# Kernel tuning notes

Measured on AMD Instinct MI355X. Metric: run time of the kernel, lower is better.

## Reference

```python
import jax, jax.numpy as jnp
import numpy as np

DIM = 768
HID = 3072
E_SPEC = 4
E_SHARED = 2
TOP_K = 2
LN_EPS = 1e-5


def _expert_stack_params(key, n_experts):
    k1, k2, k3, k4 = jax.random.split(key, 4)
    s1 = 1.0 / np.sqrt(DIM)
    s2 = 1.0 / np.sqrt(HID)
    return {
        'w1': jax.random.uniform(k1, (n_experts, DIM, HID), minval=-s1, maxval=s1, dtype=jnp.float32),
        'b1': jax.random.uniform(k2, (n_experts, HID), minval=-s1, maxval=s1, dtype=jnp.float32),
        'w2': jax.random.uniform(k3, (n_experts, HID, DIM), minval=-s2, maxval=s2, dtype=jnp.float32),
        'b2': jax.random.uniform(k4, (n_experts, DIM), minval=-s2, maxval=s2, dtype=jnp.float32),
    }


def setup_inputs() -> dict:
    key = jax.random.key(0)
    ks = jax.random.split(key, 8)
    B, N = 64, 196
    s = 1.0 / np.sqrt(DIM)
    spec = _expert_stack_params(ks[1], E_SPEC)
    shared = _expert_stack_params(ks[2], E_SHARED)
    return {
        'x': jax.random.normal(ks[0], (B, N, DIM), dtype=jnp.float32),
        'ln_gamma': jnp.ones((DIM,), jnp.float32),
        'ln_beta': jnp.zeros((DIM,), jnp.float32),
        'spec_router_w': jax.random.uniform(ks[3], (DIM, E_SPEC), minval=-s, maxval=s, dtype=jnp.float32),
        'spec_router_b': jnp.zeros((E_SPEC,), jnp.float32),
        'spec_w1': spec['w1'], 'spec_b1': spec['b1'], 'spec_w2': spec['w2'], 'spec_b2': spec['b2'],
        'shared_router_w': jax.random.uniform(ks[4], (DIM, E_SHARED), minval=-s, maxval=s, dtype=jnp.float32),
        'shared_router_b': jnp.zeros((E_SHARED,), jnp.float32),
        'sh_w1': shared['w1'], 'sh_b1': shared['b1'], 'sh_w2': shared['w2'], 'sh_b2': shared['b2'],
    }


def _all_experts(x, w1, b1, w2, b2):
    # x: [B,N,D]; w1: [E,D,H] -> out: [B,N,E,D]
    h = jnp.einsum('bnd,edh->bneh', x, w1) + b1
    h = jax.nn.gelu(h, approximate=False)  # torch nn.GELU default is exact
    return jnp.einsum('bneh,ehd->bned', h, w2) + b2


def reference(x, ln_gamma, ln_beta,
              spec_router_w, spec_router_b, spec_w1, spec_b1, spec_w2, spec_b2,
              shared_router_w, shared_router_b, sh_w1, sh_b1, sh_w2, sh_b2):
    # LayerNorm
    mu = jnp.mean(x, axis=-1, keepdims=True)
    var = jnp.mean(jnp.square(x - mu), axis=-1, keepdims=True)
    xn = (x - mu) * jax.lax.rsqrt(var + LN_EPS) * ln_gamma + ln_beta

    # Specific-expert branch: dense all-expert compute, then top-k gather (faithful)
    spec_logits = xn @ spec_router_w + spec_router_b            # [B,N,E]
    spec_probs = jax.nn.softmax(spec_logits, axis=-1)
    topk_probs, topk_idx = jax.lax.top_k(spec_probs, TOP_K)    # [B,N,K]
    spec_out_all = _all_experts(xn, spec_w1, spec_b1, spec_w2, spec_b2)  # [B,N,E,D]
    sel = jnp.take_along_axis(spec_out_all, topk_idx[..., None], axis=2)  # [B,N,K,D]
    specific_out = jnp.sum(topk_probs[..., None] * sel, axis=2)

    # Shared-expert branch: softmax-weighted sum over all experts
    sh_logits = xn @ shared_router_w + shared_router_b          # [B,N,Es]
    sh_probs = jax.nn.softmax(sh_logits, axis=-1)
    sh_out_all = _all_experts(xn, sh_w1, sh_b1, sh_w2, sh_b2)   # [B,N,Es,D]
    shared_out = jnp.einsum('bne,bned->bnd', sh_probs, sh_out_all)

    out = specific_out + shared_out
    return (out, spec_logits, spec_probs, topk_idx, topk_probs, sh_logits, sh_probs)
```

## Files before the change

kernel.cpp:

```cpp
#include <hip/hip_runtime.h>
#include <hip/hip_bf16.h>
#include <math.h>

#define NTOK 12544
#define DIM 768
#define HID 3072
#define NTILE_MAX 102
#define NSLOT_MAX (NTILE_MAX * 256)
#define NSDT 49
#define NVT (NTILE_MAX + 2 * NSDT)
#define NBKT 64
#define BKTCAP 256
#define LDSB 131072

typedef __hip_bfloat16 bf16;
typedef __attribute__((ext_vector_type(8))) short short8v;
typedef __attribute__((ext_vector_type(4))) float f32x4;

#define GPTR(p)  ((const __attribute__((address_space(1))) void*)(p))
#define LDSPTR(p) ((__attribute__((address_space(3))) void*)(p))

__global__ __launch_bounds__(256) void conv_all_kernel(
    const float* __restrict__ spec_w1, const float* __restrict__ sh_w1,
    const float* __restrict__ spec_w2, const float* __restrict__ sh_w2,
    bf16* __restrict__ w1t, bf16* __restrict__ w2t,
    int* __restrict__ cnt2, int* __restrict__ slot_tok, float* __restrict__ slot_gate) {
    int z = blockIdx.y;
    int ti = blockIdx.x;
    int t = threadIdx.x;
    if (z == 0) {
        if (ti == 0) cnt2[t] = 0;
        if (ti < NTILE_MAX) {
            int s = ti * 256 + t;
            slot_tok[s] = 0; slot_gate[s] = 0.0f;
        }
    }
    const float* src; bf16* dst; int R, C, tr, tc;
    if (z < 6) {
        R = DIM; C = HID;
        src = (z < 4) ? spec_w1 + (size_t)z * R * C : sh_w1 + (size_t)(z - 4) * R * C;
        dst = w1t + (size_t)z * R * C;
        tr = ti % 12; tc = ti / 12;
    } else {
        int e = z - 6;
        R = HID; C = DIM;
        src = (e < 4) ? spec_w2 + (size_t)e * R * C : sh_w2 + (size_t)(e - 4) * R * C;
        dst = w2t + (size_t)e * R * C;
        tr = ti % 48; tc = ti / 48;
    }
    __shared__ float tile[64][65];
    int r0 = tr * 64, c0 = tc * 64;
    int lr = t >> 4, lc = (t & 15) * 4;
    #pragma unroll
    for (int ii = 0; ii < 4; ++ii) {
        float4 v = *(const float4*)&src[(size_t)(r0 + lr + 16 * ii) * C + c0 + lc];
        tile[lc + 0][lr + 16 * ii] = v.x;
        tile[lc + 1][lr + 16 * ii] = v.y;
        tile[lc + 2][lr + 16 * ii] = v.z;
        tile[lc + 3][lr + 16 * ii] = v.w;
    }
    __syncthreads();
    int oc = t >> 4, orr = (t & 15) * 4;
    #pragma unroll
    for (int ii = 0; ii < 4; ++ii) {
        union { ushort4 u4; bf16 h[4]; } pk;
        #pragma unroll
        for (int k = 0; k < 4; ++k)
            pk.h[k] = __float2bfloat16(tile[oc + 16 * ii][orr + k]);
        *(ushort4*)&dst[(size_t)(c0 + oc + 16 * ii) * R + r0 + orr] = pk.u4;
    }
}

__global__ void router_ln_kernel(const float* __restrict__ x,
                                 const float* __restrict__ lng, const float* __restrict__ lnb,
                                 const float* __restrict__ srw, const float* __restrict__ srb,
                                 const float* __restrict__ shw, const float* __restrict__ shb,
                                 bf16* __restrict__ xnb,
                                 float* __restrict__ spec_logits, float* __restrict__ spec_probs,
                                 float* __restrict__ topk_idx, float* __restrict__ topk_probs,
                                 float* __restrict__ sh_logits, float* __restrict__ sh_probs,
                                 float* __restrict__ gates,
                                 int* __restrict__ cnt2, int* __restrict__ tok2,
                                 float* __restrict__ gate2) {
    int t = blockIdx.x * 4 + (threadIdx.x >> 6);
    int bucket = blockIdx.x & (NBKT - 1);
    int lane = threadIdx.x & 63;
    const float* xr = x + (size_t)t * DIM;
    bf16* xb = xnb + (size_t)t * DIM;
    float v[12];
    float s = 0.0f;
    #pragma unroll
    for (int i = 0; i < 6; ++i) {
        float2 xv = *(const float2*)&xr[lane * 2 + 128 * i];
        v[2 * i] = xv.x; v[2 * i + 1] = xv.y;
        s += xv.x + xv.y;
    }
    #pragma unroll
    for (int o = 32; o > 0; o >>= 1) s += __shfl_xor(s, o, 64);
    float mean = s * (1.0f / 768.0f);
    float sq = 0.0f;
    #pragma unroll
    for (int i = 0; i < 12; ++i) { float d = v[i] - mean; sq += d * d; }
    #pragma unroll
    for (int o = 32; o > 0; o >>= 1) sq += __shfl_xor(sq, o, 64);
    float rstd = rsqrtf(sq * (1.0f / 768.0f) + 1e-5f);

    float acc[6] = {0, 0, 0, 0, 0, 0};
    #pragma unroll
    for (int i = 0; i < 6; ++i) {
        int d0 = lane * 2 + 128 * i;
        float xn0 = (v[2 * i]     - mean) * rstd * lng[d0]     + lnb[d0];
        float xn1 = (v[2 * i + 1] - mean) * rstd * lng[d0 + 1] + lnb[d0 + 1];
        union { unsigned u; bf16 h[2]; } pk;
        pk.h[0] = __float2bfloat16(xn0);
        pk.h[1] = __float2bfloat16(xn1);
        *(unsigned*)&xb[d0] = pk.u;
        float4 a = *(const float4*)&srw[d0 * 4];
        float4 b = *(const float4*)&srw[d0 * 4 + 4];
        acc[0] += xn0 * a.x + xn1 * b.x;
        acc[1] += xn0 * a.y + xn1 * b.y;
        acc[2] += xn0 * a.z + xn1 * b.z;
        acc[3] += xn0 * a.w + xn1 * b.w;
        float4 sw = *(const float4*)&shw[d0 * 2];
        acc[4] += xn0 * sw.x + xn1 * sw.z;
        acc[5] += xn0 * sw.y + xn1 * sw.w;
    }
    #pragma unroll
    for (int j = 0; j < 6; ++j) {
        #pragma unroll
        for (int o = 32; o > 0; o >>= 1) acc[j] += __shfl_xor(acc[j], o, 64);
    }
    if (lane == 0) {
        float l[4];
        #pragma unroll
        for (int j = 0; j < 4; ++j) l[j] = acc[j] + srb[j];
        float m = fmaxf(fmaxf(l[0], l[1]), fmaxf(l[2], l[3]));
        float e[4], ssum = 0.0f;
        #pragma unroll
        for (int j = 0; j < 4; ++j) { e[j] = expf(l[j] - m); ssum += e[j]; }
        float inv = 1.0f / ssum;
        float p[4];
        #pragma unroll
        for (int j = 0; j < 4; ++j) p[j] = e[j] * inv;
        int i0 = 0;
        for (int j = 1; j < 4; ++j) if (p[j] > p[i0]) i0 = j;
        int i1 = -1;
        for (int j = 0; j < 4; ++j) {
            if (j == i0) continue;
            if (i1 < 0 || p[j] > p[i1]) i1 = j;
        }
        float sl0 = acc[4] + shb[0], sl1 = acc[5] + shb[1];
        float sm = fmaxf(sl0, sl1);
        float se0 = expf(sl0 - sm), se1 = expf(sl1 - sm);
        float sinv = 1.0f / (se0 + se1);
        float sp0 = se0 * sinv, sp1 = se1 * sinv;

        #pragma unroll
        for (int j = 0; j < 4; ++j) {
            spec_logits[t * 4 + j] = l[j];
            spec_probs[t * 4 + j]  = p[j];
        }
        topk_idx[t * 2 + 0]   = (float)i0;
        topk_idx[t * 2 + 1]   = (float)i1;
        topk_probs[t * 2 + 0] = p[i0];
        topk_probs[t * 2 + 1] = p[i1];
        sh_logits[t * 2 + 0]  = sl0;
        sh_logits[t * 2 + 1]  = sl1;
        sh_probs[t * 2 + 0]   = sp0;
        sh_probs[t * 2 + 1]   = sp1;
        float gg[6] = {0, 0, 0, 0, sp0, sp1};
        gg[i0] = p[i0];
        gg[i1] = p[i1];
        #pragma unroll
        for (int j = 0; j < 6; ++j) gates[t * 6 + j] = gg[j];
        int c0 = i0 * NBKT + bucket;
        int pos0 = atomicAdd(&cnt2[c0], 1);
        tok2[c0 * BKTCAP + pos0]  = t * 2 + 0;
        gate2[c0 * BKTCAP + pos0] = p[i0];
        int c1 = i1 * NBKT + bucket;
        int pos1 = atomicAdd(&cnt2[c1], 1);
        tok2[c1 * BKTCAP + pos1]  = t * 2 + 1;
        gate2[c1 * BKTCAP + pos1] = p[i1];
    }
}

__global__ void plan_kernel(const int* __restrict__ cnt2, int* __restrict__ e_of_tile,
                            const int* __restrict__ tok2, const float* __restrict__ gate2,
                            int* __restrict__ slot_tok, float* __restrict__ slot_gate,
                            int* __restrict__ back) {
    __shared__ int sbase[4 * NBKT];
    __shared__ int offsE[5];
    __shared__ int etot[4];
    int tid = threadIdx.x, lane = tid & 63, wid = tid >> 6;
    int c = cnt2[wid * NBKT + lane];
    int inc = c;
    #pragma unroll
    for (int o = 1; o < 64; o <<= 1) {
        int tv = __shfl_up(inc, o, 64);
        if (lane >= o) inc += tv;
    }
    int exc = inc - c;
    if (lane == 63) etot[wid] = inc;
    __syncthreads();
    if (tid == 0) {
        int o = 0;
        for (int e = 0; e < 4; ++e) { offsE[e] = o; o += (etot[e] + 255) & ~255; }
        offsE[4] = o;
    }
    __syncthreads();
    sbase[tid] = offsE[wid] + exc;
    for (int idx = tid; idx < NTILE_MAX; idx += 256) {
        int s0 = idx * 256, e = -1;
        for (int j = 0; j < 4; ++j)
            if (s0 >= offsE[j] && s0 < offsE[j + 1]) e = j;
        e_of_tile[idx] = e;
    }
    __syncthreads();
    int bs = sbase[tid];
    int cc = cnt2[tid];
    for (int i = 0; i < cc; ++i) {
        int gs = bs + i;
        int tk = tok2[tid * BKTCAP + i];
        slot_tok[gs] = tk >> 1;
        slot_gate[gs] = gate2[tid * BKTCAP + i];
        back[tk] = gs;
    }
}


__device__ __forceinline__ int swz(int off) {
    return off ^ (((off >> 8) & 1) << 4) ^ (((off >> 9) & 1) << 5);
}

__device__ __forceinline__ void stage2(bf16* lds, int base_elems, int wid,
                                       const bf16* s0, const bf16* s1) {
    __builtin_amdgcn_global_load_lds(GPTR(s0), LDSPTR(lds + base_elems + wid * 512), 16, 0, 0);
    __builtin_amdgcn_global_load_lds(GPTR(s1), LDSPTR(lds + base_elems + 4096 + wid * 512), 16, 0, 0);
}

__device__ __forceinline__ void read_a4(const bf16* lds, int buf, int ks, int wm, int mh,
                                        int lane, short8v a[4]) {
    const char* base = (const char*)lds + buf * 32768 + ks * 16384;
    #pragma unroll
    for (int i = 0; i < 4; ++i) {
        int off = (wm * 128 + mh * 64 + i * 16 + (lane & 15)) * 64 + ((lane >> 4) * 16);
        a[i] = *(const short8v*)(base + swz(off));
    }
}

__device__ __forceinline__ void read_b4(const bf16* lds, int buf, int ks, int wn,
                                        int lane, short8v b[4]) {
    const char* base = (const char*)lds + 65536 + buf * 32768 + ks * 16384;
    #pragma unroll
    for (int j = 0; j < 4; ++j) {
        int off = (wn * 64 + j * 16 + (lane & 15)) * 64 + ((lane >> 4) * 16);
        b[j] = *(const short8v*)(base + swz(off));
    }
}

__device__ __forceinline__ void mfma16(const short8v a[4], const short8v b[4], f32x4 (*am)[4]) {
    #pragma unroll
    for (int i = 0; i < 4; ++i)
        #pragma unroll
        for (int j = 0; j < 4; ++j)
            am[i][j] = __builtin_amdgcn_mfma_f32_16x16x32_bf16(a[i], b[j], am[i][j], 0, 0, 0);
}

#define BARRIER() __builtin_amdgcn_s_barrier()
#define VMCNT4() asm volatile("s_waitcnt vmcnt(4)" ::: "memory")
#define VMCNT0() asm volatile("s_waitcnt vmcnt(0)" ::: "memory")

template<int NT>
__device__ __forceinline__ void kloop8p(bf16* lds, const bf16* a0, const bf16* a1,
                                        const bf16* b0, const bf16* b1,
                                        int wm, int wn, int wid, int lane,
                                        f32x4 acc[8][4]) {
    stage2(lds, 0, wid, a0, a1);
    stage2(lds, 32768, wid, b0, b1);
    stage2(lds, 8192, wid, a0 + 32, a1 + 32);
    stage2(lds, 32768 + 8192, wid, b0 + 32, b1 + 32);
    VMCNT4();
    BARRIER();
    for (int t = 0; t < NT; ++t) {
        int buf = t & 1, nb = buf ^ 1;
        bool pre = (t + 1 < NT);
        short8v af[4], bfv[4];
        if (pre) stage2(lds, nb * 16384, wid, a0 + (t + 1) * 64, a1 + (t + 1) * 64);
        read_a4(lds, buf, 0, wm, 0, lane, af);
        read_b4(lds, buf, 0, wn, lane, bfv);
        BARRIER();
        __builtin_amdgcn_s_setprio(1);
        mfma16(af, bfv, &acc[0]);
        __builtin_amdgcn_s_setprio(0);
        BARRIER();
        if (pre) stage2(lds, 32768 + nb * 16384, wid, b0 + (t + 1) * 64, b1 + (t + 1) * 64);
        read_a4(lds, buf, 0, wm, 1, lane, af);
        BARRIER();
        __builtin_amdgcn_s_setprio(1);
        mfma16(af, bfv, &acc[4]);
        __builtin_amdgcn_s_setprio(0);
        if (pre) VMCNT4(); else VMCNT0();
        BARRIER();
        if (pre) stage2(lds, nb * 16384 + 8192, wid, a0 + (t + 1) * 64 + 32, a1 + (t + 1) * 64 + 32);
        read_a4(lds, buf, 1, wm, 0, lane, af);
        read_b4(lds, buf, 1, wn, lane, bfv);
        BARRIER();
        __builtin_amdgcn_s_setprio(1);
        mfma16(af, bfv, &acc[0]);
        __builtin_amdgcn_s_setprio(0);
        BARRIER();
        if (pre) stage2(lds, 32768 + nb * 16384 + 8192, wid, b0 + (t + 1) * 64 + 32, b1 + (t + 1) * 64 + 32);
        read_a4(lds, buf, 1, wm, 1, lane, af);
        BARRIER();
        __builtin_amdgcn_s_setprio(1);
        mfma16(af, bfv, &acc[4]);
        __builtin_amdgcn_s_setprio(0);
        if (pre) VMCNT4();
        BARRIER();
    }
}

__device__ __forceinline__ float gelu_exact(float v) {
    return 0.5f * v * (1.0f + erff(v * 0.70710678118654752f));
}

__global__ __launch_bounds__(512, 2) void gemm1_8p(
    const bf16* __restrict__ xnb, const bf16* __restrict__ w1t,
    const float* __restrict__ spec_b1, const float* __restrict__ sh_b1,
    const int* __restrict__ e_of_tile, const int* __restrict__ slot_tok,
    bf16* __restrict__ Hbuf, int y_base) {
    extern __shared__ bf16 lds[];
    int y = blockIdx.y + y_base;
    int tid = threadIdx.x, wid = tid >> 6, lane = tid & 63;
    int wm = wid >> 2, wn = wid & 3;
    int P0c = tid, P1c = 512 + tid;
    int L0 = P0c ^ ((P0c >> 4) & 1) ^ (((P0c >> 5) & 1) << 1);
    int L1 = P1c ^ ((P1c >> 4) & 1) ^ (((P1c >> 5) & 1) << 1);
    int r0 = L0 >> 2, c0 = (L0 & 3) * 8;
    int r1 = L1 >> 2, c1 = (L1 & 3) * 8;

    const bf16 *a0, *a1, *Bw;
    const float* bias;
    if (y < NTILE_MAX) {
        int e = e_of_tile[y];
        if (e < 0) return;
        a0 = xnb + (size_t)slot_tok[y * 256 + r0] * DIM + c0;
        a1 = xnb + (size_t)slot_tok[y * 256 + r1] * DIM + c1;
        Bw = w1t + (size_t)e * HID * DIM;
        bias = spec_b1 + (size_t)e * HID;
    } else {
        int ys = y - NTILE_MAX;
        int z = ys / NSDT, ry = ys % NSDT;
        a0 = xnb + (size_t)(ry * 256 + r0) * DIM + c0;
        a1 = xnb + (size_t)(ry * 256 + r1) * DIM + c1;
        Bw = w1t + (size_t)(4 + z) * HID * DIM;
        bias = sh_b1 + (size_t)z * HID;
    }
    const bf16* b0 = Bw + (size_t)(blockIdx.x * 256 + r0) * DIM + c0;
    const bf16* b1 = Bw + (size_t)(blockIdx.x * 256 + r1) * DIM + c1;

    f32x4 acc[8][4] = {};
    kloop8p<DIM / 64>(lds, a0, a1, b0, b1, wm, wn, wid, lane, acc);

    bf16* hb = Hbuf + (size_t)blockIdx.y * 256 * HID;
    int fr = lane & 15, fq = lane >> 4;
    int cb = blockIdx.x * 256 + wn * 64;
    #pragma unroll
    for (int j = 0; j < 4; ++j) {
        int col = cb + j * 16 + fr;
        float bv = bias[col];
        #pragma unroll
        for (int ii = 0; ii < 8; ++ii) {
            #pragma unroll
            for (int rr = 0; rr < 4; ++rr) {
                int row = wm * 128 + (ii >> 2) * 64 + (ii & 3) * 16 + fq * 4 + rr;
                hb[(size_t)row * HID + col] = __float2bfloat16(gelu_exact(acc[ii][j][rr] + bv));
            }
        }
    }
}

__global__ __launch_bounds__(512, 2) void gemm2_8p(
    const bf16* __restrict__ Hbuf, const bf16* __restrict__ w2t,
    const float* __restrict__ spec_b2, const float* __restrict__ sh_b2,
    const int* __restrict__ e_of_tile, const float* __restrict__ slot_gate,
    const float* __restrict__ sh_probs,
    bf16* __restrict__ spec_g, bf16* __restrict__ shg, int y_base) {
    extern __shared__ bf16 lds[];
    int y = blockIdx.y + y_base;
    int tid = threadIdx.x, wid = tid >> 6, lane = tid & 63;
    int wm = wid >> 2, wn = wid & 3;
    int P0c = tid, P1c = 512 + tid;
    int L0 = P0c ^ ((P0c >> 4) & 1) ^ (((P0c >> 5) & 1) << 1);
    int L1 = P1c ^ ((P1c >> 4) & 1) ^ (((P1c >> 5) & 1) << 1);
    int r0 = L0 >> 2, c0 = (L0 & 3) * 8;
    int r1 = L1 >> 2, c1 = (L1 & 3) * 8;

    const bf16 *Bw;
    const float* bias;
    bf16* obase;
    bool grouped = (y < NTILE_MAX);
    int z = 0, ry = 0;
    if (grouped) {
        int e = e_of_tile[y];
        if (e < 0) return;
        Bw = w2t + (size_t)e * DIM * HID;
        bias = spec_b2 + (size_t)e * DIM;
        obase = spec_g + (size_t)y * 256 * DIM;
    } else {
        int ys = y - NTILE_MAX;
        z = ys / NSDT; ry = ys % NSDT;
        Bw = w2t + (size_t)(4 + z) * DIM * HID;
        bias = sh_b2 + (size_t)z * DIM;
        obase = shg + (size_t)(z * NTOK + ry * 256) * DIM;
    }
    const bf16* Ah = Hbuf + (size_t)blockIdx.y * 256 * HID;
    const bf16* a0 = Ah + (size_t)r0 * HID + c0;
    const bf16* a1 = Ah + (size_t)r1 * HID + c1;
    const bf16* b0 = Bw + (size_t)(blockIdx.x * 256 + r0) * HID + c0;
    const bf16* b1 = Bw + (size_t)(blockIdx.x * 256 + r1) * HID + c1;

    f32x4 acc[8][4] = {};
    kloop8p<HID / 64>(lds, a0, a1, b0, b1, wm, wn, wid, lane, acc);

    int fr = lane & 15, fq = lane >> 4;
    int cb = blockIdx.x * 256 + wn * 64;
    #pragma unroll
    for (int j = 0; j < 4; ++j) {
        int col = cb + j * 16 + fr;
        float bv = bias[col];
        #pragma unroll
        for (int ii = 0; ii < 8; ++ii) {
            #pragma unroll
            for (int rr = 0; rr < 4; ++rr) {
                int row = wm * 128 + (ii >> 2) * 64 + (ii & 3) * 16 + fq * 4 + rr;
                float g = grouped ? slot_gate[y * 256 + row]
                                  : sh_probs[(size_t)(ry * 256 + row) * 2 + z];
                obase[(size_t)row * DIM + col] = __float2bfloat16(g * (acc[ii][j][rr] + bv));
            }
        }
    }
}

__device__ __forceinline__ void stage_tile(const bf16* __restrict__ g, int ldg,
                                           bf16* lds, int tid) {
    int wave = tid >> 6, lane = tid & 63;
    #pragma unroll
    for (int q = 0; q < 2; ++q) {
        int chunk = wave * 2 + q;
        int row = chunk * 16 + (lane >> 2);
        int col = (lane & 3) * 8;
        __builtin_amdgcn_global_load_lds(GPTR(g + (size_t)row * ldg + col),
                                         LDSPTR(lds + chunk * 512), 16, 0, 0);
    }
}

__device__ __forceinline__ void mfma_step(const bf16* As, const bf16* Bs,
                                          int wr, int wc, int fr, int fq, f32x4 acc[4][4]) {
    short8v a[4], b[4];
    #pragma unroll
    for (int i = 0; i < 4; ++i) {
        a[i] = *(const short8v*)&As[(wr * 64 + i * 16 + fr) * 32 + fq * 8];
        b[i] = *(const short8v*)&Bs[(wc * 64 + i * 16 + fr) * 32 + fq * 8];
    }
    #pragma unroll
    for (int i = 0; i < 4; ++i)
        #pragma unroll
        for (int j = 0; j < 4; ++j)
            acc[i][j] = __builtin_amdgcn_mfma_f32_16x16x32_bf16(a[i], b[j], acc[i][j], 0, 0, 0);
}

__global__ __launch_bounds__(256) void gemm1_dense(
    const bf16* __restrict__ A, const bf16* __restrict__ BT,
    const float* __restrict__ bias, bf16* __restrict__ H) {
    __shared__ bf16 As[128 * 32];
    __shared__ bf16 Bs[128 * 32];
    int tid = threadIdx.x;
    int wid = tid >> 6, lane = tid & 63;
    int wr = wid >> 1, wc = wid & 1;
    int fr = lane & 15, fq = lane >> 4;
    const bf16* Ag = A + (size_t)(blockIdx.y * 128) * DIM;
    const bf16* Bg = BT + (size_t)(blockIdx.x * 128) * DIM;
    f32x4 acc[4][4] = {};
    for (int k0 = 0; k0 < DIM; k0 += 32) {
        stage_tile(Ag + k0, DIM, As, tid);
        stage_tile(Bg + k0, DIM, Bs, tid);
        __syncthreads();
        mfma_step(As, Bs, wr, wc, fr, fq, acc);
        __syncthreads();
    }
    int rbase = blockIdx.y * 128 + wr * 64;
    int cbase = blockIdx.x * 128 + wc * 64;
    #pragma unroll
    for (int j = 0; j < 4; ++j) {
        int col = cbase + j * 16 + fr;
        float bv = bias[col];
        #pragma unroll
        for (int i = 0; i < 4; ++i)
            #pragma unroll
            for (int r = 0; r < 4; ++r) {
                int row = rbase + i * 16 + fq * 4 + r;
                H[(size_t)row * HID + col] = __float2bfloat16(gelu_exact(acc[i][j][r] + bv));
            }
    }
}

__global__ __launch_bounds__(256) void gemm2_dense_out(
    const bf16* __restrict__ A, const bf16* __restrict__ BT,
    const float* __restrict__ bias, const float* __restrict__ gates,
    float* __restrict__ out, int gidx, int accum) {
    __shared__ bf16 As[128 * 32];
    __shared__ bf16 Bs[128 * 32];
    int tid = threadIdx.x;
    int wid = tid >> 6, lane = tid & 63;
    int wr = wid >> 1, wc = wid & 1;
    int fr = lane & 15, fq = lane >> 4;
    const bf16* Ag = A + (size_t)(blockIdx.y * 128) * HID;
    const bf16* Bg = BT + (size_t)(blockIdx.x * 128) * HID;
    f32x4 acc[4][4] = {};
    for (int k0 = 0; k0 < HID; k0 += 32) {
        stage_tile(Ag + k0, HID, As, tid);
        stage_tile(Bg + k0, HID, Bs, tid);
        __syncthreads();
        mfma_step(As, Bs, wr, wc, fr, fq, acc);
        __syncthreads();
    }
    int rbase = blockIdx.y * 128 + wr * 64;
    int cbase = blockIdx.x * 128 + wc * 64;
    #pragma unroll
    for (int j = 0; j < 4; ++j) {
        int col = cbase + j * 16 + fr;
        float bv = bias[col];
        #pragma unroll
        for (int i = 0; i < 4; ++i)
            #pragma unroll
            for (int r = 0; r < 4; ++r) {
                int row = rbase + i * 16 + fq * 4 + r;
                float g = gates[(size_t)row * 6 + gidx];
                float v = g * (acc[i][j][r] + bv);
                size_t idx = (size_t)row * DIM + col;
                out[idx] = accum ? out[idx] + v : v;
            }
    }
}

__global__ void combine_kernel(const bf16* __restrict__ spec_g, const bf16* __restrict__ shg,
                               const int* __restrict__ back, float* __restrict__ out) {
    int idx = blockIdx.x * 256 + threadIdx.x;
    int tok = idx / 96;
    int c = (idx % 96) * 8;
    int b0 = back[2 * tok], b1 = back[2 * tok + 1];
    short8v q0 = *(const short8v*)&spec_g[(size_t)b0 * DIM + c];
    short8v q1 = *(const short8v*)&spec_g[(size_t)b1 * DIM + c];
    short8v s0 = *(const short8v*)&shg[(size_t)tok * DIM + c];
    short8v s1 = *(const short8v*)&shg[(size_t)(NTOK + tok) * DIM + c];
    float o[8];
    #pragma unroll
    for (int k = 0; k < 8; ++k) {
        float f0 = __uint_as_float((unsigned)(unsigned short)q0[k] << 16);
        float f1 = __uint_as_float((unsigned)(unsigned short)q1[k] << 16);
        float f2 = __uint_as_float((unsigned)(unsigned short)s0[k] << 16);
        float f3 = __uint_as_float((unsigned)(unsigned short)s1[k] << 16);
        o[k] = f0 + f1 + f2 + f3;
    }
    float* op = out + (size_t)tok * DIM + c;
    *(float4*)(op)     = *(const float4*)(o);
    *(float4*)(op + 4) = *(const float4*)(o + 4);
}

static inline size_t align256(size_t x) { return (x + 255) & ~(size_t)255; }

extern "C" void kernel_launch(void* const* d_in, const int* in_sizes, int n_in,
                              void* d_out, int out_size, void* d_ws, size_t ws_size,
                              hipStream_t stream) {
    const float* x      = (const float*)d_in[0];
    const float* gamma  = (const float*)d_in[1];
    const float* beta   = (const float*)d_in[2];
    const float* srw    = (const float*)d_in[3];
    const float* srb    = (const float*)d_in[4];
    const float* spec_w1 = (const float*)d_in[5];
    const float* spec_b1 = (const float*)d_in[6];
    const float* spec_w2 = (const float*)d_in[7];
    const float* spec_b2 = (const float*)d_in[8];
    const float* shw    = (const float*)d_in[9];
    const float* shb    = (const float*)d_in[10];
    const float* sh_w1  = (const float*)d_in[11];
    const float* sh_b1  = (const float*)d_in[12];
    const float* sh_w2  = (const float*)d_in[13];
    const float* sh_b2  = (const float*)d_in[14];

    char* p = (char*)d_ws;
    size_t off = 0;
    bf16* xnb = (bf16*)(p + off);       off = align256(off + (size_t)NTOK * DIM * 2);
    bf16* w1t = (bf16*)(p + off);       off = align256(off + (size_t)6 * HID * DIM * 2);
    bf16* w2t = (bf16*)(p + off);       off = align256(off + (size_t)6 * DIM * HID * 2);
    int*  cnt2 = (int*)(p + off);       off = align256(off + (size_t)4 * NBKT * 4);
    float* gates = (float*)(p + off);   off = align256(off + (size_t)NTOK * 6 * 4);
    int*  tok2 = (int*)(p + off);       off = align256(off + (size_t)4 * NBKT * BKTCAP * 4);
    float* gate2 = (float*)(p + off);   off = align256(off + (size_t)4 * NBKT * BKTCAP * 4);
    int*  slot_tok = (int*)(p + off);   off = align256(off + (size_t)NSLOT_MAX * 4);
    float* slot_gate = (float*)(p + off); off = align256(off + (size_t)NSLOT_MAX * 4);
    int*  back = (int*)(p + off);       off = align256(off + (size_t)2 * NTOK * 4);
    int*  e_of_tile = (int*)(p + off);  off = align256(off + (size_t)NTILE_MAX * 4);
    bf16* spec_g = (bf16*)(p + off);    off = align256(off + (size_t)NSLOT_MAX * DIM * 2);
    bf16* shg   = (bf16*)(p + off);     off = align256(off + (size_t)2 * NTOK * DIM * 2);
    size_t fixed_end = off;
    bf16* Hbuf = (bf16*)(p + fixed_end);

    const size_t tile_bytes = (size_t)256 * HID * 2;
    size_t avail = (ws_size > fixed_end) ? (ws_size - fixed_end) : 0;
    int tcap = (int)(avail / tile_bytes);
    if (tcap > NVT) tcap = NVT;

    float* out         = (float*)d_out;
    float* spec_logits = out + (size_t)NTOK * DIM;
    float* spec_probs  = spec_logits + (size_t)NTOK * 4;
    float* topk_idx    = spec_probs  + (size_t)NTOK * 4;
    float* topk_probs  = topk_idx    + (size_t)NTOK * 2;
    float* sh_logits   = topk_probs  + (size_t)NTOK * 2;
    float* sh_probs    = sh_logits   + (size_t)NTOK * 2;

    conv_all_kernel<<<dim3(576, 12), 256, 0, stream>>>(
        spec_w1, sh_w1, spec_w2, sh_w2, w1t, w2t, cnt2, slot_tok, slot_gate);

    router_ln_kernel<<<NTOK / 4, 256, 0, stream>>>(x, gamma, beta, srw, srb, shw, shb, xnb,
                                                   spec_logits, spec_probs, topk_idx,
                                                   topk_probs, sh_logits, sh_probs, gates,
                                                   cnt2, tok2, gate2);

    if (tcap >= 16) {
        plan_kernel<<<1, 256, 0, stream>>>(cnt2, e_of_tile, tok2, gate2,
                                           slot_tok, slot_gate, back);
        for (int c0 = 0; c0 < NVT; c0 += tcap) {
            int n = NVT - c0 < tcap ? NVT - c0 : tcap;
            gemm1_8p<<<dim3(HID / 256, n), 512, LDSB, stream>>>(
                xnb, w1t, spec_b1, sh_b1, e_of_tile, slot_tok, Hbuf, c0);
            gemm2_8p<<<dim3(DIM / 256, n), 512, LDSB, stream>>>(
                Hbuf, w2t, spec_b2, sh_b2, e_of_tile, slot_gate, sh_probs,
                spec_g, shg, c0);
        }
        combine_kernel<<<NTOK * 96 / 256, 256, 0, stream>>>(spec_g, shg, back, out);
    } else {
        bf16* HB = spec_g;
        for (int e = 0; e < 6; ++e) {
            const bf16* w1p = w1t + (size_t)e * HID * DIM;
            const bf16* w2p = w2t + (size_t)e * DIM * HID;
            const float* b1p = (e < 4) ? spec_b1 + (size_t)e * HID : sh_b1 + (size_t)(e - 4) * HID;
            const float* b2p = (e < 4) ? spec_b2 + (size_t)e * DIM : sh_b2 + (size_t)(e - 4) * DIM;
            gemm1_dense<<<dim3(HID / 128, NTOK / 128), 256, 0, stream>>>(xnb, w1p, b1p, HB);
            gemm2_dense_out<<<dim3(DIM / 128, NTOK / 128), 256, 0, stream>>>(
                HB, w2p, b2p, gates, out, e, e > 0);
        }
    }
}
```

Measured before the change: 930.2 us.

## Pre-gather routed tokens, remap blocks across XCDs, use polynomial GELU

```diff
diff --git a/kernel.cpp b/kernel.cpp
--- a/kernel.cpp
+++ b/kernel.cpp
@@ -227,6 +227,14 @@
     }
 }
 
+__global__ void gather_kernel(const bf16* __restrict__ xnb, const int* __restrict__ slot_tok,
+                              bf16* __restrict__ xg) {
+    int idx = blockIdx.x * 256 + threadIdx.x;
+    int slot = idx / 96;
+    int c = (idx % 96) * 8;
+    int tok = slot_tok[slot];
+    *(short8v*)&xg[(size_t)slot * DIM + c] = *(const short8v*)&xnb[(size_t)tok * DIM + c];
+}
 
 __device__ __forceinline__ int swz(int off) {
     return off ^ (((off >> 8) & 1) << 4) ^ (((off >> 9) & 1) << 5);
@@ -324,13 +332,35 @@
     return 0.5f * v * (1.0f + erff(v * 0.70710678118654752f));
 }
 
+__device__ __forceinline__ float gelu_fast(float x) {
+    float z = 0.70710678118654752f * x;
+    float az = fabsf(z);
+    float t = __builtin_amdgcn_rcpf(1.0f + 0.3275911f * az);
+    float poly = t * (0.254829592f + t * (-0.284496736f + t * (1.421413741f +
+                 t * (-1.453152027f + t * 1.061405429f))));
+    float erfv = 1.0f - poly * __expf(-az * az);
+    erfv = (z < 0.0f) ? -erfv : erfv;
+    return 0.5f * x * (1.0f + erfv);
+}
+
+__device__ __forceinline__ void xcd_remap(int& bx, int& by) {
+    int nx = gridDim.x, nwg = nx * gridDim.y;
+    int flat = blockIdx.y * nx + blockIdx.x;
+    int q = nwg >> 3, r = nwg & 7;
+    int xcd = flat & 7, lid = flat >> 3;
+    int f2 = (xcd < r ? xcd * (q + 1) : r * (q + 1) + (xcd - r) * q) + lid;
+    bx = f2 % nx; by = f2 / nx;
+}
+
 __global__ __launch_bounds__(512, 2) void gemm1_8p(
-    const bf16* __restrict__ xnb, const bf16* __restrict__ w1t,
+    const bf16* __restrict__ xg, const bf16* __restrict__ xnb,
+    const bf16* __restrict__ w1t,
     const float* __restrict__ spec_b1, const float* __restrict__ sh_b1,
-    const int* __restrict__ e_of_tile, const int* __restrict__ slot_tok,
+    const int* __restrict__ e_of_tile,
     bf16* __restrict__ Hbuf, int y_base) {
     extern __shared__ bf16 lds[];
-    int y = blockIdx.y + y_base;
+    int bx, by; xcd_remap(bx, by);
+    int y = by + y_base;
     int tid = threadIdx.x, wid = tid >> 6, lane = tid & 63;
     int wm = wid >> 2, wn = wid & 3;
     int P0c = tid, P1c = 512 + tid;
@@ -339,32 +369,32 @@
     int r0 = L0 >> 2, c0 = (L0 & 3) * 8;
     int r1 = L1 >> 2, c1 = (L1 & 3) * 8;
 
-    const bf16 *a0, *a1, *Bw;
+    const bf16 *abase, *Bw;
     const float* bias;
     if (y < NTILE_MAX) {
         int e = e_of_tile[y];
         if (e < 0) return;
-        a0 = xnb + (size_t)slot_tok[y * 256 + r0] * DIM + c0;
-        a1 = xnb + (size_t)slot_tok[y * 256 + r1] * DIM + c1;
+        abase = xg + (size_t)y * 256 * DIM;
         Bw = w1t + (size_t)e * HID * DIM;
         bias = spec_b1 + (size_t)e * HID;
     } else {
         int ys = y - NTILE_MAX;
         int z = ys / NSDT, ry = ys % NSDT;
-        a0 = xnb + (size_t)(ry * 256 + r0) * DIM + c0;
-        a1 = xnb + (size_t)(ry * 256 + r1) * DIM + c1;
+        abase = xnb + (size_t)ry * 256 * DIM;
         Bw = w1t + (size_t)(4 + z) * HID * DIM;
         bias = sh_b1 + (size_t)z * HID;
     }
-    const bf16* b0 = Bw + (size_t)(blockIdx.x * 256 + r0) * DIM + c0;
-    const bf16* b1 = Bw + (size_t)(blockIdx.x * 256 + r1) * DIM + c1;
+    const bf16* a0 = abase + (size_t)r0 * DIM + c0;
+    const bf16* a1 = abase + (size_t)r1 * DIM + c1;
+    const bf16* b0 = Bw + (size_t)(bx * 256 + r0) * DIM + c0;
+    const bf16* b1 = Bw + (size_t)(bx * 256 + r1) * DIM + c1;
 
     f32x4 acc[8][4] = {};
     kloop8p<DIM / 64>(lds, a0, a1, b0, b1, wm, wn, wid, lane, acc);
 
-    bf16* hb = Hbuf + (size_t)blockIdx.y * 256 * HID;
+    bf16* hb = Hbuf + (size_t)by * 256 * HID;
     int fr = lane & 15, fq = lane >> 4;
-    int cb = blockIdx.x * 256 + wn * 64;
+    int cb = bx * 256 + wn * 64;
     #pragma unroll
     for (int j = 0; j < 4; ++j) {
         int col = cb + j * 16 + fr;
@@ -374,7 +404,7 @@
             #pragma unroll
             for (int rr = 0; rr < 4; ++rr) {
                 int row = wm * 128 + (ii >> 2) * 64 + (ii & 3) * 16 + fq * 4 + rr;
-                hb[(size_t)row * HID + col] = __float2bfloat16(gelu_exact(acc[ii][j][rr] + bv));
+                hb[(size_t)row * HID + col] = __float2bfloat16(gelu_fast(acc[ii][j][rr] + bv));
             }
         }
     }
@@ -387,7 +417,8 @@
     const float* __restrict__ sh_probs,
     bf16* __restrict__ spec_g, bf16* __restrict__ shg, int y_base) {
     extern __shared__ bf16 lds[];
-    int y = blockIdx.y + y_base;
+    int bx, by; xcd_remap(bx, by);
+    int y = by + y_base;
     int tid = threadIdx.x, wid = tid >> 6, lane = tid & 63;
     int wm = wid >> 2, wn = wid & 3;
     int P0c = tid, P1c = 512 + tid;
@@ -414,17 +445,17 @@
         bias = sh_b2 + (size_t)z * DIM;
         obase = shg + (size_t)(z * NTOK + ry * 256) * DIM;
     }
-    const bf16* Ah = Hbuf + (size_t)blockIdx.y * 256 * HID;
+    const bf16* Ah = Hbuf + (size_t)by * 256 * HID;
     const bf16* a0 = Ah + (size_t)r0 * HID + c0;
     const bf16* a1 = Ah + (size_t)r1 * HID + c1;
-    const bf16* b0 = Bw + (size_t)(blockIdx.x * 256 + r0) * HID + c0;
-    const bf16* b1 = Bw + (size_t)(blockIdx.x * 256 + r1) * HID + c1;
+    const bf16* b0 = Bw + (size_t)(bx * 256 + r0) * HID + c0;
+    const bf16* b1 = Bw + (size_t)(bx * 256 + r1) * HID + c1;
 
     f32x4 acc[8][4] = {};
     kloop8p<HID / 64>(lds, a0, a1, b0, b1, wm, wn, wid, lane, acc);
 
     int fr = lane & 15, fq = lane >> 4;
-    int cb = blockIdx.x * 256 + wn * 64;
+    int cb = bx * 256 + wn * 64;
     #pragma unroll
     for (int j = 0; j < 4; ++j) {
         int col = cb + j * 16 + fr;
@@ -604,6 +635,7 @@
     int*  e_of_tile = (int*)(p + off);  off = align256(off + (size_t)NTILE_MAX * 4);
     bf16* spec_g = (bf16*)(p + off);    off = align256(off + (size_t)NSLOT_MAX * DIM * 2);
     bf16* shg   = (bf16*)(p + off);     off = align256(off + (size_t)2 * NTOK * DIM * 2);
+    bf16* xg    = (bf16*)(p + off);     off = align256(off + (size_t)NSLOT_MAX * DIM * 2);
     size_t fixed_end = off;
     bf16* Hbuf = (bf16*)(p + fixed_end);
 
@@ -628,13 +660,14 @@
                                                    topk_probs, sh_logits, sh_probs, gates,
                                                    cnt2, tok2, gate2);
 
-    if (tcap >= 16) {
+    if (tcap >= 8) {
         plan_kernel<<<1, 256, 0, stream>>>(cnt2, e_of_tile, tok2, gate2,
                                            slot_tok, slot_gate, back);
+        gather_kernel<<<NSLOT_MAX * 96 / 256, 256, 0, stream>>>(xnb, slot_tok, xg);
         for (int c0 = 0; c0 < NVT; c0 += tcap) {
             int n = NVT - c0 < tcap ? NVT - c0 : tcap;
             gemm1_8p<<<dim3(HID / 256, n), 512, LDSB, stream>>>(
-                xnb, w1t, spec_b1, sh_b1, e_of_tile, slot_tok, Hbuf, c0);
+                xg, xnb, w1t, spec_b1, sh_b1, e_of_tile, Hbuf, c0);
             gemm2_8p<<<dim3(DIM / 256, n), 512, LDSB, stream>>>(
                 Hbuf, w2t, spec_b2, sh_b2, e_of_tile, slot_gate, sh_probs,
                 spec_g, shg, c0);
```

Measured after the change: 1.123 ms. 20.7% more time.
